# Kernel tuning notes

Measured on AMD Instinct MI355X. Metric: run time of the kernel, lower is better.

Reference implementation:

```python
import jax, jax.numpy as jnp
import numpy as np

ROPE_BASE = 10000.0
NEG_INF = -1e9


def _rope_tables(L, dh, dtype):
    # standard RoPE: inv_freq over half dims, tables shaped [L, dh]
    half = dh // 2
    inv_freq = 1.0 / (ROPE_BASE ** (jnp.arange(0, half, dtype=jnp.float32) * 2.0 / dh))
    freqs = jnp.arange(L, dtype=jnp.float32)[:, None] * inv_freq[None, :]  # [L, half]
    emb = jnp.concatenate([freqs, freqs], axis=-1)  # [L, dh]
    return jnp.cos(emb).astype(dtype), jnp.sin(emb).astype(dtype)


def _apply_rope(t, cos, sin):
    # t: [B, H, L, dh]; rotate-half convention
    dh = t.shape[-1]
    t1, t2 = t[..., : dh // 2], t[..., dh // 2:]
    rot = jnp.concatenate([-t2, t1], axis=-1)
    return t * cos[None, None] + rot * sin[None, None]


def setup_inputs() -> dict:
    key = jax.random.key(0)
    ks = jax.random.split(key, 7)
    B, L, D, nh = 2, 2048, 2048, 16
    s = 0.02
    return {
        "x": jax.random.normal(ks[0], (B, L, D), dtype=jnp.float32),
        "Wq": jax.random.normal(ks[1], (D, 2 * D), dtype=jnp.float32) * s,
        "Wk": jax.random.normal(ks[2], (D, D), dtype=jnp.float32) * s,
        "Wv": jax.random.normal(ks[3], (D, D), dtype=jnp.float32) * s,
        "Wl": jax.random.normal(ks[4], (D, nh), dtype=jnp.float32) * s,
        "bl": jnp.zeros((nh,), dtype=jnp.float32),
        "Wo": jax.random.normal(ks[5], (D, D), dtype=jnp.float32) * s,
    }


def reference(x, Wq, Wk, Wv, Wl, bl, Wo):
    B, L, D = x.shape
    nh = Wl.shape[1]
    dh = D // nh

    q = (x @ Wq).reshape(B, L, 2 * nh, dh).transpose(0, 2, 1, 3)  # [B, 2nh, L, dh]
    k = (x @ Wk).reshape(B, L, nh, dh).transpose(0, 2, 1, 3)      # [B, nh, L, dh]
    v = (x @ Wv).reshape(B, L, nh, dh).transpose(0, 2, 1, 3)      # [B, nh, L, dh]

    cos, sin = _rope_tables(L, dh, x.dtype)
    q = _apply_rope(q, cos, sin)
    k = _apply_rope(k, cos, sin)

    # pair query heads (2i, 2i+1) share k/v head i — avoid repeat_interleave
    qp = q.reshape(B, nh, 2, L, dh)
    scale = 1.0 / jnp.sqrt(jnp.asarray(dh, dtype=x.dtype))
    scores = jnp.einsum("bhpqd,bhkd->bhpqk", qp, k) * scale  # [B, nh, 2, L, L]
    causal = jnp.tril(jnp.ones((L, L), dtype=bool))
    scores = jnp.where(causal[None, None, None], scores, NEG_INF)
    probs = jax.nn.softmax(scores, axis=-1)
    ctx = jnp.einsum("bhpqk,bhkd->bhpqd", probs, v)  # [B, nh, 2, L, dh]

    lam = jax.nn.sigmoid(x @ Wl + bl).transpose(0, 2, 1)[..., None]  # [B, nh, L, 1]
    out = ctx[:, :, 0] - lam * ctx[:, :, 1]  # [B, nh, L, dh]
    out = out.transpose(0, 2, 1, 3).reshape(B, L, D)
    return out @ Wo
```

## Files before the change

kernel.cpp:

```cpp
#include <hip/hip_runtime.h>
#include <cstddef>
#include <cstdint>

#define L_SEQ 2048
#define D_MODEL 2048
#define NH 16
#define DH 128
#define M_ROWS 4096

__device__ __forceinline__ ushort f2bf(float f) {
    union { float f; uint32_t u; } v; v.f = f;
    const uint32_t u = v.u;
    return (ushort)((u + 0x7fffu + ((u >> 16) & 1u)) >> 16);
}
__device__ __forceinline__ float bf2f(ushort h) {
    union { uint32_t u; float f; } v; v.u = ((uint32_t)h) << 16; return v.f;
}
__device__ __forceinline__ float2 bf2f2(uint32_t u) {
    union { uint32_t u; float f; } lo, hi;
    lo.u = u << 16; hi.u = u & 0xffff0000u;
    return make_float2(lo.f, hi.f);
}

__device__ __forceinline__ void gld_lds16(const void* g, void* l) {
    __builtin_amdgcn_global_load_lds(
        (const __attribute__((address_space(1))) void*)g,
        (__attribute__((address_space(3))) void*)l, 16, 0, 0);
}

typedef __bf16  bf16x8 __attribute__((ext_vector_type(8)));
typedef float   f32x4  __attribute__((ext_vector_type(4)));

__global__ __launch_bounds__(256) void cvt_bf16(
    const float* __restrict__ in, ushort* __restrict__ out)
{
    const int i = (blockIdx.x * 256 + threadIdx.x) * 8;
    const float4 a = *(const float4*)&in[i];
    const float4 b = *(const float4*)&in[i + 4];
    uint4 o;
    o.x = (uint)f2bf(a.x) | ((uint)f2bf(a.y) << 16);
    o.y = (uint)f2bf(a.z) | ((uint)f2bf(a.w) << 16);
    o.z = (uint)f2bf(b.x) | ((uint)f2bf(b.y) << 16);
    o.w = (uint)f2bf(b.z) | ((uint)f2bf(b.w) << 16);
    *(uint4*)&out[i] = o;
}

__global__ __launch_bounds__(256) void transpose_cvt(
    const float* __restrict__ W, ushort* __restrict__ Wt, int K, int N)
{
    __shared__ float tile[32][33];
    const int n0 = blockIdx.x * 32, k0 = blockIdx.y * 32;
    const int t = threadIdx.x;
    const int r = t >> 3;
    const int c4 = (t & 7) * 4;
    const float4 v = *(const float4*)&W[(size_t)(k0 + r) * N + n0 + c4];
    tile[r][c4 + 0] = v.x; tile[r][c4 + 1] = v.y;
    tile[r][c4 + 2] = v.z; tile[r][c4 + 3] = v.w;
    __syncthreads();
    ushort4 o;
    o.x = f2bf(tile[c4 + 0][r]);
    o.y = f2bf(tile[c4 + 1][r]);
    o.z = f2bf(tile[c4 + 2][r]);
    o.w = f2bf(tile[c4 + 3][r]);
    *(ushort4*)&Wt[(size_t)(n0 + r) * K + k0 + c4] = o;
}

__global__ __launch_bounds__(256) void rope_table(float2* __restrict__ tab)
{
    const int i = blockIdx.x * 256 + threadIdx.x;
    const int d = i & 63, l = i >> 6;
    const float inv = exp2f(-(float)d * 0.20762050593045857f);
    const float ang = (float)l * inv;
    float s, c;
    sincosf(ang, &s, &c);
    tab[i] = make_float2(c, s);
}

__global__ __launch_bounds__(256) void rope_k(
    ushort* __restrict__ T, const float2* __restrict__ tab)
{
    const int idx = blockIdx.x * 256 + threadIdx.x;
    const int d2   = (idx & 31) * 2;
    const int head = (idx >> 5) & 15;
    const int row  = idx >> 9;
    const int l    = row & (L_SEQ - 1);
    const size_t base = (size_t)row * 2048 + head * 128 + d2;
    const uint a = *(const uint*)&T[base];
    const uint b = *(const uint*)&T[base + 64];
    const float2 t0 = bf2f2(a);
    const float2 t1 = bf2f2(b);
    const float2 cs0 = tab[l * 64 + d2];
    const float2 cs1 = tab[l * 64 + d2 + 1];
    const float o0x = t0.x * cs0.x - t1.x * cs0.y;
    const float o0y = t0.y * cs1.x - t1.y * cs1.y;
    const float o1x = t1.x * cs0.x + t0.x * cs0.y;
    const float o1y = t1.y * cs1.x + t0.y * cs1.y;
    *(uint*)&T[base]      = (uint)f2bf(o0x) | ((uint)f2bf(o0y) << 16);
    *(uint*)&T[base + 64] = (uint)f2bf(o1x) | ((uint)f2bf(o1y) << 16);
}

template <int MODE>
__global__ __launch_bounds__(256) void gemm_bf16(
    const ushort* __restrict__ A, const ushort* __restrict__ Bt,
    void* __restrict__ Cv, int M, int N, int K)
{
    __shared__ __align__(16) ushort As[128 * 32];
    __shared__ __align__(16) ushort Bs[128 * 32];
    const int bm = blockIdx.y * 128;
    const int bn = blockIdx.x * 128;
    const int t = threadIdx.x;
    const int w = t >> 6, lane = t & 63;
    const int wm = (w & 1) * 64;
    const int wn = (w >> 1) * 64;

    const int srow = t >> 2;
    const int scol = (t & 3) * 8;
    const ushort* Ag  = A  + (size_t)(bm + srow) * K + scol;
    const ushort* Ag2 = A  + (size_t)(bm + 64 + srow) * K + scol;
    const ushort* Bg  = Bt + (size_t)(bn + srow) * K + scol;
    const ushort* Bg2 = Bt + (size_t)(bn + 64 + srow) * K + scol;
    ushort* Asl  = &As[(size_t)t * 8];
    ushort* Asl2 = &As[(size_t)(t + 256) * 8];
    ushort* Bsl  = &Bs[(size_t)t * 8];
    ushort* Bsl2 = &Bs[(size_t)(t + 256) * 8];

    const int fr = lane & 15;
    const int fq = (lane >> 4) * 8;
    const ushort* Abase = &As[(size_t)(wm + fr) * 32 + fq];
    const ushort* Bbase = &Bs[(size_t)(wn + fr) * 32 + fq];

    f32x4 acc[4][4] = {};

    for (int k0 = 0; k0 < K; k0 += 32) {
        __syncthreads();
        gld_lds16(Ag + k0, Asl);
        gld_lds16(Ag2 + k0, Asl2);
        gld_lds16(Bg + k0, Bsl);
        gld_lds16(Bg2 + k0, Bsl2);
        __syncthreads();
        bf16x8 a[4], b[4];
        #pragma unroll
        for (int i = 0; i < 4; ++i) {
            a[i] = *(const bf16x8*)(Abase + (size_t)i * 16 * 32);
            b[i] = *(const bf16x8*)(Bbase + (size_t)i * 16 * 32);
        }
        #pragma unroll
        for (int mt = 0; mt < 4; ++mt)
            #pragma unroll
            for (int nt = 0; nt < 4; ++nt)
                acc[mt][nt] = __builtin_amdgcn_mfma_f32_16x16x32_bf16(
                    a[mt], b[nt], acc[mt][nt], 0, 0, 0);
    }

    const int crow = (lane >> 4) * 4;
    const int ccol = lane & 15;
    #pragma unroll
    for (int mt = 0; mt < 4; ++mt) {
        #pragma unroll
        for (int nt = 0; nt < 4; ++nt) {
            if (MODE == 3) {
                const size_t row = bm + wm + mt * 16 + crow;
                const size_t col = bn + wn + nt * 16 + ccol;
                ushort4 o4;
                o4.x = f2bf(acc[mt][nt][0]); o4.y = f2bf(acc[mt][nt][1]);
                o4.z = f2bf(acc[mt][nt][2]); o4.w = f2bf(acc[mt][nt][3]);
                *(ushort4*)&((ushort*)Cv)[
                    ((row >> 11) * 16 + (col >> 7)) * (size_t)(128 * 2048)
                    + (col & 127) * 2048 + (row & 2047)] = o4;
            } else {
                #pragma unroll
                for (int reg = 0; reg < 4; ++reg) {
                    const size_t row = bm + wm + mt * 16 + crow + reg;
                    const size_t col = bn + wn + nt * 16 + ccol;
                    if (MODE == 1) {
                        ((ushort*)Cv)[row * N + col] = f2bf(acc[mt][nt][reg]);
                    } else {
                        ((float*)Cv)[row * N + col] = acc[mt][nt][reg];
                    }
                }
            }
        }
    }
}

__global__ __launch_bounds__(256) void lam_kernel(
    const float* __restrict__ X, const float* __restrict__ Wl,
    const float* __restrict__ bl, float* __restrict__ Lam)
{
    const int idx = blockIdx.x * 256 + threadIdx.x;
    const int hh  = idx & 15;
    const int m   = idx >> 4;
    const float* xr = X + (size_t)m * D_MODEL;
    float acc = 0.0f;
    for (int d = 0; d < D_MODEL; d += 4) {
        const float4 xv = *(const float4*)&xr[d];
        acc += xv.x * Wl[(d + 0) * NH + hh];
        acc += xv.y * Wl[(d + 1) * NH + hh];
        acc += xv.z * Wl[(d + 2) * NH + hh];
        acc += xv.w * Wl[(d + 3) * NH + hh];
    }
    acc += bl[hh];
    Lam[idx] = 1.0f / (1.0f + expf(-acc));
}

__global__ __launch_bounds__(256, 2) void attn_mfma(
    const ushort* __restrict__ Qb, const ushort* __restrict__ Kb,
    const ushort* __restrict__ Vtg, const float* __restrict__ Lam,
    const float2* __restrict__ Rtab, ushort* __restrict__ OutB)
{
    __shared__ __align__(16) ushort lds[27136];
    ushort* K_sh  = lds;
    ushort* Vt_sh = lds + 8704;
    ushort* P_sh  = lds + 17920;

    const int h  = blockIdx.y;
    const int b  = blockIdx.z;
    const int pt = blockIdx.x;
    const int t  = threadIdx.x;
    const int w = t >> 6, lane = t & 63;
    const int colL = lane & 15, quad = lane >> 4;
    const int p = w >> 1, slot = w & 1;
    ushort* Pw = P_sh + w * (32 * 72);

    const ushort* Kgbase = Kb  + (size_t)(b * 2048) * 2048 + h * 128;
    const ushort* Vgbase = Vtg + (size_t)((b * 16 + h) * 128) * 2048;
    const float scale2 = 0.12751744f;

    for (int ph = 0; ph < 2; ++ph) {
        const int qt  = ph ? pt : 31 - pt;
        const int q0  = qt * 64;
        const int r0w = q0 + slot * 32;

        bf16x8 qf[2][4];
        #pragma unroll
        for (int g = 0; g < 2; ++g) {
            const int l = r0w + g * 16 + colL;
            const ushort* Qr = Qb + (size_t)(b * 2048 + l) * 4096
                             + (2 * h + p) * 128 + quad * 8;
            ushort raw[4][8];
            #pragma unroll
            for (int c = 0; c < 4; ++c)
                *(uint4*)raw[c] = *(const uint4*)&Qr[c * 32];
            const float2* tb = Rtab + l * 64 + quad * 8;
            ushort o[4][8];
            #pragma unroll
            for (int c = 0; c < 2; ++c)
                #pragma unroll
                for (int j = 0; j < 8; ++j) {
                    const float2 cs = tb[c * 32 + j];
                    const float a  = bf2f(raw[c][j]);
                    const float bb = bf2f(raw[c + 2][j]);
                    o[c][j]     = f2bf(a * cs.x - bb * cs.y);
                    o[c + 2][j] = f2bf(bb * cs.x + a * cs.y);
                }
            #pragma unroll
            for (int c = 0; c < 4; ++c)
                qf[g][c] = *(const bf16x8*)o[c];
        }

        f32x4 ctx[2][8] = {};
        float m2[2][4] = {{-1e30f,-1e30f,-1e30f,-1e30f},
                          {-1e30f,-1e30f,-1e30f,-1e30f}};
        float li[2][4] = {};

        for (int kt = 0; kt <= qt; ++kt) {
            const int kt0 = kt * 64;
            __syncthreads();
            {
                uint4 kvr[4], vvr[4];
                #pragma unroll
                for (int i = 0; i < 4; ++i) {
                    const int c = t + i * 256;
                    kvr[i] = *(const uint4*)&Kgbase[(size_t)(kt0 + (c >> 4)) * 2048 + (c & 15) * 8];
                    vvr[i] = *(const uint4*)&Vgbase[(size_t)(c >> 3) * 2048 + kt0 + (c & 7) * 8];
                }
                #pragma unroll
                for (int i = 0; i < 4; ++i) {
                    const int c = t + i * 256;
                    *(uint4*)&K_sh[(c >> 4) * 136 + (c & 15) * 8] = kvr[i];
                    *(uint4*)&Vt_sh[(c >> 3) * 72 + (c & 7) * 8]  = vvr[i];
                }
            }
            __syncthreads();

            f32x4 sc2[2][4] = {};
            __builtin_amdgcn_s_setprio(1);
            #pragma unroll
            for (int c = 0; c < 4; ++c)
                #pragma unroll
                for (int nt = 0; nt < 4; ++nt) {
                    const bf16x8 kf = *(const bf16x8*)
                        &K_sh[(nt * 16 + colL) * 136 + c * 32 + quad * 8];
                    sc2[0][nt] = __builtin_amdgcn_mfma_f32_16x16x32_bf16(
                        qf[0][c], kf, sc2[0][nt], 0, 0, 0);
                    sc2[1][nt] = __builtin_amdgcn_mfma_f32_16x16x32_bf16(
                        qf[1][c], kf, sc2[1][nt], 0, 0, 0);
                }
            __builtin_amdgcn_s_setprio(0);

            const bool dmask = (kt == qt);
            #pragma unroll
            for (int g = 0; g < 2; ++g)
                #pragma unroll
                for (int reg = 0; reg < 4; ++reg) {
                    const int row = r0w + g * 16 + quad * 4 + reg;
                    float s[4];
                    #pragma unroll
                    for (int nt = 0; nt < 4; ++nt) {
                        float v = sc2[g][nt][reg] * scale2;
                        if (dmask && (kt0 + nt * 16 + colL > row)) v = -1e9f;
                        s[nt] = v;
                    }
                    float mx = fmaxf(fmaxf(s[0], s[1]), fmaxf(s[2], s[3]));
                    #pragma unroll
                    for (int off = 8; off >= 1; off >>= 1)
                        mx = fmaxf(mx, __shfl_xor(mx, off));
                    const float mnew  = fmaxf(m2[g][reg], mx);
                    const float alpha = exp2f(m2[g][reg] - mnew);
                    float rs = 0.f;
                    #pragma unroll
                    for (int nt = 0; nt < 4; ++nt) {
                        const float pv = exp2f(s[nt] - mnew);
                        s[nt] = pv;
                        rs += pv;
                    }
                    #pragma unroll
                    for (int off = 8; off >= 1; off >>= 1)
                        rs += __shfl_xor(rs, off);
                    li[g][reg] = li[g][reg] * alpha + rs;
                    m2[g][reg] = mnew;
                    #pragma unroll
                    for (int nt2 = 0; nt2 < 8; ++nt2)
                        ctx[g][nt2][reg] *= alpha;
                    #pragma unroll
                    for (int nt = 0; nt < 4; ++nt)
                        Pw[(g * 16 + quad * 4 + reg) * 72 + nt * 16 + colL]
                            = f2bf(s[nt]);
                }

            __builtin_amdgcn_s_setprio(1);
            #pragma unroll
            for (int c2 = 0; c2 < 2; ++c2) {
                const bf16x8 pf0 = *(const bf16x8*)
                    &Pw[colL * 72 + c2 * 32 + quad * 8];
                const bf16x8 pf1 = *(const bf16x8*)
                    &Pw[(16 + colL) * 72 + c2 * 32 + quad * 8];
                #pragma unroll
                for (int nt2 = 0; nt2 < 8; ++nt2) {
                    const bf16x8 vf = *(const bf16x8*)
                        &Vt_sh[(nt2 * 16 + colL) * 72 + c2 * 32 + quad * 8];
                    ctx[0][nt2] = __builtin_amdgcn_mfma_f32_16x16x32_bf16(
                        pf0, vf, ctx[0][nt2], 0, 0, 0);
                    ctx[1][nt2] = __builtin_amdgcn_mfma_f32_16x16x32_bf16(
                        pf1, vf, ctx[1][nt2], 0, 0, 0);
                }
            }
            __builtin_amdgcn_s_setprio(0);
        }

        float invl[2][4];
        #pragma unroll
        for (int g = 0; g < 2; ++g)
            #pragma unroll
            for (int reg = 0; reg < 4; ++reg)
                invl[g][reg] = 1.0f / li[g][reg];

        float* comb = (float*)lds;
        __syncthreads();
        if (p == 1) {
            #pragma unroll
            for (int g = 0; g < 2; ++g)
                #pragma unroll
                for (int nt2 = 0; nt2 < 8; ++nt2)
                    #pragma unroll
                    for (int reg = 0; reg < 4; ++reg)
                        comb[(slot * 32 + g * 16 + quad * 4 + reg) * 130
                             + nt2 * 16 + colL] = ctx[g][nt2][reg] * invl[g][reg];
        }
        __syncthreads();
        if (p == 0) {
            #pragma unroll
            for (int g = 0; g < 2; ++g)
                #pragma unroll
                for (int reg = 0; reg < 4; ++reg) {
                    const int row = r0w + g * 16 + quad * 4 + reg;
                    const float lamv = Lam[(size_t)(b * 2048 + row) * 16 + h];
                    ushort* orow = OutB + (size_t)(b * 2048 + row) * 2048 + h * 128;
                    #pragma unroll
                    for (int nt2 = 0; nt2 < 8; ++nt2) {
                        const float c1 = comb[(slot * 32 + g * 16 + quad * 4 + reg) * 130
                                              + nt2 * 16 + colL];
                        const float o = ctx[g][nt2][reg] * invl[g][reg] - lamv * c1;
                        orow[nt2 * 16 + colL] = f2bf(o);
                    }
                }
        }
        __syncthreads();
    }
}

extern "C" void kernel_launch(void* const* d_in, const int* in_sizes, int n_in,
                              void* d_out, int out_size, void* d_ws, size_t ws_size,
                              hipStream_t stream)
{
    const float* x  = (const float*)d_in[0];
    const float* Wq = (const float*)d_in[1];
    const float* Wk = (const float*)d_in[2];
    const float* Wv = (const float*)d_in[3];
    const float* Wl = (const float*)d_in[4];
    const float* bl = (const float*)d_in[5];
    const float* Wo = (const float*)d_in[6];
    float* out = (float*)d_out;
    (void)ws_size; (void)in_sizes; (void)n_in; (void)out_size;

    ushort* ws   = (ushort*)d_ws;
    ushort* xb   = ws;
    ushort* Qb16 = xb   + (size_t)8388608;
    ushort* Kb16 = Qb16 + (size_t)16777216;
    ushort* Vtg  = Kb16 + (size_t)8388608;
    ushort* Wqt  = Vtg  + (size_t)8388608;
    ushort* Wkt  = Wqt  + (size_t)8388608;
    ushort* Wvt  = Wkt  + (size_t)4194304;
    ushort* Wot  = Wvt  + (size_t)4194304;
    ushort* OutB = Wot  + (size_t)4194304;
    float*  LamB = (float*)(OutB + (size_t)8388608);
    float2* Rtab = (float2*)(LamB + (size_t)65536);

    cvt_bf16<<<4096, 256, 0, stream>>>(x, xb);
    transpose_cvt<<<dim3(128, 64), 256, 0, stream>>>(Wq, Wqt, 2048, 4096);
    transpose_cvt<<<dim3(64, 64), 256, 0, stream>>>(Wk, Wkt, 2048, 2048);
    transpose_cvt<<<dim3(64, 64), 256, 0, stream>>>(Wv, Wvt, 2048, 2048);
    transpose_cvt<<<dim3(64, 64), 256, 0, stream>>>(Wo, Wot, 2048, 2048);
    lam_kernel<<<256, 256, 0, stream>>>(x, Wl, bl, LamB);
    rope_table<<<512, 256, 0, stream>>>(Rtab);

    gemm_bf16<1><<<dim3(32, 32), 256, 0, stream>>>(xb, Wqt, Qb16, M_ROWS, 4096, D_MODEL);
    gemm_bf16<1><<<dim3(16, 32), 256, 0, stream>>>(xb, Wkt, Kb16, M_ROWS, D_MODEL, D_MODEL);
    gemm_bf16<3><<<dim3(16, 32), 256, 0, stream>>>(xb, Wvt, Vtg, M_ROWS, D_MODEL, D_MODEL);

    rope_k<<<8192, 256, 0, stream>>>(Kb16, Rtab);

    attn_mfma<<<dim3(16, NH, 2), 256, 0, stream>>>(Qb16, Kb16, Vtg, LamB, Rtab, OutB);

    gemm_bf16<0><<<dim3(16, 32), 256, 0, stream>>>(OutB, Wot, out, M_ROWS, D_MODEL, D_MODEL);
}
```

Before: 665.7 us.

## Skip lazy softmax rescaling, split lam reduction, use native bf16 convert

The online-softmax rescale of the context accumulators is skipped unless the new row max exceeds the running max by more than a threshold (wave-uniform via __any), which removes most alpha multiplies in the attention inner loop. The lam projection now splits each dot product over four lanes with a shuffle reduction and launches four times as many threads, for more parallelism. f2bf is replaced by the compiler's native __bf16 conversion. The lazy rescale lets probabilities grow up to 2^11 before renormalising, which adds some risk of precision loss in bf16 P and the fp32 accumulators.

After: 720.3 us. 1.08x slower.

```diff
diff --git a/kernel.cpp b/kernel.cpp
--- a/kernel.cpp
+++ b/kernel.cpp
@@ -9,9 +9,7 @@
 #define M_ROWS 4096
 
 __device__ __forceinline__ ushort f2bf(float f) {
-    union { float f; uint32_t u; } v; v.f = f;
-    const uint32_t u = v.u;
-    return (ushort)((u + 0x7fffu + ((u >> 16) & 1u)) >> 16);
+    union { __bf16 b; ushort u; } v; v.b = (__bf16)f; return v.u;
 }
 __device__ __forceinline__ float bf2f(ushort h) {
     union { uint32_t u; float f; } v; v.u = ((uint32_t)h) << 16; return v.f;
@@ -187,20 +185,26 @@
     const float* __restrict__ X, const float* __restrict__ Wl,
     const float* __restrict__ bl, float* __restrict__ Lam)
 {
-    const int idx = blockIdx.x * 256 + threadIdx.x;
-    const int hh  = idx & 15;
-    const int m   = idx >> 4;
-    const float* xr = X + (size_t)m * D_MODEL;
+    const int idx  = blockIdx.x * 256 + threadIdx.x;
+    const int part = idx & 3;
+    const int hh   = (idx >> 2) & 15;
+    const int m    = idx >> 6;
+    const float* xr = X + (size_t)m * D_MODEL + part * 512;
+    const float* wl = Wl + (size_t)(part * 512) * NH + hh;
     float acc = 0.0f;
-    for (int d = 0; d < D_MODEL; d += 4) {
+    for (int d = 0; d < 512; d += 4) {
         const float4 xv = *(const float4*)&xr[d];
-        acc += xv.x * Wl[(d + 0) * NH + hh];
-        acc += xv.y * Wl[(d + 1) * NH + hh];
-        acc += xv.z * Wl[(d + 2) * NH + hh];
-        acc += xv.w * Wl[(d + 3) * NH + hh];
+        acc += xv.x * wl[(d + 0) * NH];
+        acc += xv.y * wl[(d + 1) * NH];
+        acc += xv.z * wl[(d + 2) * NH];
+        acc += xv.w * wl[(d + 3) * NH];
     }
-    acc += bl[hh];
-    Lam[idx] = 1.0f / (1.0f + expf(-acc));
+    acc += __shfl_xor(acc, 1);
+    acc += __shfl_xor(acc, 2);
+    if (part == 0) {
+        acc += bl[hh];
+        Lam[(size_t)m * NH + hh] = 1.0f / (1.0f + expf(-acc));
+    }
 }
 
 __global__ __launch_bounds__(256, 2) void attn_mfma(
@@ -315,23 +319,26 @@
                     #pragma unroll
                     for (int off = 8; off >= 1; off >>= 1)
                         mx = fmaxf(mx, __shfl_xor(mx, off));
-                    const float mnew  = fmaxf(m2[g][reg], mx);
-                    const float alpha = exp2f(m2[g][reg] - mnew);
+                    if (__any(mx > m2[g][reg] + 11.0f)) {
+                        const float mnew  = fmaxf(m2[g][reg], mx);
+                        const float alpha = exp2f(m2[g][reg] - mnew);
+                        li[g][reg] *= alpha;
+                        m2[g][reg] = mnew;
+                        #pragma unroll
+                        for (int nt2 = 0; nt2 < 8; ++nt2)
+                            ctx[g][nt2][reg] *= alpha;
+                    }
                     float rs = 0.f;
                     #pragma unroll
                     for (int nt = 0; nt < 4; ++nt) {
-                        const float pv = exp2f(s[nt] - mnew);
+                        const float pv = exp2f(s[nt] - m2[g][reg]);
                         s[nt] = pv;
                         rs += pv;
                     }
                     #pragma unroll
                     for (int off = 8; off >= 1; off >>= 1)
                         rs += __shfl_xor(rs, off);
-                    li[g][reg] = li[g][reg] * alpha + rs;
-                    m2[g][reg] = mnew;
-                    #pragma unroll
-                    for (int nt2 = 0; nt2 < 8; ++nt2)
-                        ctx[g][nt2][reg] *= alpha;
+                    li[g][reg] += rs;
                     #pragma unroll
                     for (int nt = 0; nt < 4; ++nt)
                         Pw[(g * 16 + quad * 4 + reg) * 72 + nt * 16 + colL]
@@ -431,7 +438,7 @@
     transpose_cvt<<<dim3(64, 64), 256, 0, stream>>>(Wk, Wkt, 2048, 2048);
     transpose_cvt<<<dim3(64, 64), 256, 0, stream>>>(Wv, Wvt, 2048, 2048);
     transpose_cvt<<<dim3(64, 64), 256, 0, stream>>>(Wo, Wot, 2048, 2048);
-    lam_kernel<<<256, 256, 0, stream>>>(x, Wl, bl, LamB);
+    lam_kernel<<<1024, 256, 0, stream>>>(x, Wl, bl, LamB);
     rope_table<<<512, 256, 0, stream>>>(Rtab);
 
     gemm_bf16<1><<<dim3(32, 32), 256, 0, stream>>>(xb, Wqt, Qb16, M_ROWS, 4096, D_MODEL);
```
